# Kernel tuning notes

Hardware: AMD Instinct MI355X
Metric: run time of the kernel (lower is better)

## Reference

```python
import jax, jax.numpy as jnp
import numpy as np

MARGIN = 0.5

def setup_inputs() -> dict:
    key = jax.random.key(0)
    k1, k2 = jax.random.split(key)
    inputs = jax.random.normal(k1, (8192, 256), dtype=jnp.float32)
    target = jax.random.randint(k2, (8192,), 0, 100, dtype=jnp.int64)
    return {"inputs": inputs, "target": target}

def reference(inputs, target):
    N = inputs.shape[0]
    # pairwise squared distances via ||xi||^2 + ||xj||^2 - 2 xi.xj
    sq = jnp.sum(inputs * inputs, axis=1)  # [N]
    gram = inputs @ inputs.T               # [N, N]
    distance = sq[:, None] + sq[None, :] - 2.0 * gram  # [N, N]
    R = (target[None, :] == target[:, None]).astype(inputs.dtype)  # [N, N]
    loss = R * distance + (1.0 - R) * jnp.maximum(MARGIN - distance, 0.0)
    return jnp.sum(loss) / (N * (N - 1.0) * 2.0)
```

## Files before the change

kernel.cpp:

```cpp
#include <hip/hip_runtime.h>
#include <stdint.h>

#define N      8192
#define KDIM   256
#define BM     128
#define TILES  (N / BM)
#define NPAIRS (TILES * (TILES + 1) / 2)
#define MARGIN 0.5f
#define PLANE  ((size_t)N * 128)

typedef float     f32x4 __attribute__((ext_vector_type(4)));
typedef long long i64x2 __attribute__((ext_vector_type(2)));

__device__ __forceinline__ void async_copy16(const void* g, void* l) {
    __builtin_amdgcn_global_load_lds(
        (__attribute__((address_space(1))) void*)(g),
        (__attribute__((address_space(3))) void*)(l),
        16, 0, 0);
}

#if !__has_builtin(__builtin_amdgcn_cvt_pk_fp8_f32)
__device__ __forceinline__ uint32_t f2e4m3(float f) {
    uint32_t u = __float_as_uint(f);
    uint32_t s = (u >> 24) & 0x80u;
    uint32_t au = u & 0x7fffffffu;
    if (au == 0) return s;
    int32_t  exp = (int32_t)(au >> 23) - 127;
    uint32_t man = (au & 0x7fffffu) | 0x800000u;
    uint32_t code;
    if (exp >= -6) {
        code = (uint32_t)((exp + 7) << 3) | ((man >> 20) & 7u);
        uint32_t rem = man & 0xFFFFFu;
        if (rem > 0x80000u || (rem == 0x80000u && (code & 1u))) code++;
    } else {
        int shift = 14 - exp;
        if (shift > 24) return s;
        code = man >> shift;
        uint32_t rem = man & ((1u << shift) - 1u);
        uint32_t h = 1u << (shift - 1);
        if (rem > h || (rem == h && (code & 1u))) code++;
    }
    return s | code;
}
__device__ __forceinline__ uint32_t pack_fp8x4(float4 v) {
    return f2e4m3(v.x) | (f2e4m3(v.y) << 8) | (f2e4m3(v.z) << 16) |
           (f2e4m3(v.w) << 24);
}
#else
__device__ __forceinline__ uint32_t pack_fp8x4(float4 v) {
    int pk = __builtin_amdgcn_cvt_pk_fp8_f32(v.x, v.y, 0, false);
    pk = __builtin_amdgcn_cvt_pk_fp8_f32(v.z, v.w, pk, true);
    return (uint32_t)pk;
}
#endif

__global__ __launch_bounds__(256) void prep_kernel(
        const float* __restrict__ X, uint8_t* __restrict__ Xq,
        float* __restrict__ sq) {
    int row  = blockIdx.x * 4 + (threadIdx.x >> 6);
    int lane = threadIdx.x & 63;

    float4 v = *((const float4*)(X + (size_t)row * KDIM) + lane);
    float ss = v.x * v.x + v.y * v.y + v.z * v.z + v.w * v.w;
    uint32_t pk = pack_fp8x4(v);

    int kg = lane * 4;
    int h  = kg >> 7;
    int kh = kg & 127;
    int ks = kh >> 5;
    int fq = (kh >> 3) & 3;
    int slot = (fq * 2 + (ks >> 1)) ^ (row & 7);
    size_t off = (size_t)h * PLANE + (size_t)row * 128
               + slot * 16 + (ks & 1) * 8 + (kh & 4);
    *(uint32_t*)(Xq + off) = pk;

    #pragma unroll
    for (int o = 32; o > 0; o >>= 1) ss += __shfl_down(ss, o, 64);
    if (lane == 0) sq[row] = ss;
}

__device__ __forceinline__ void compute_half(
        const uint8_t* aB, const uint8_t* bB, int fquad, int key,
        f32x4 (&acc)[4][4]) {
    #pragma unroll
    for (int ks2 = 0; ks2 < 2; ++ks2) {
        const int t = ((fquad * 2 + ks2) ^ key) * 16;
        i64x2 a2[4], b2[4];
        #pragma unroll
        for (int im = 0; im < 4; ++im)
            a2[im] = *(const i64x2*)(aB + im * 16 * 128 + t);
        #pragma unroll
        for (int in = 0; in < 4; ++in)
            b2[in] = *(const i64x2*)(bB + in * 16 * 128 + t);
        #pragma unroll
        for (int im = 0; im < 4; ++im)
            #pragma unroll
            for (int in = 0; in < 4; ++in)
                acc[im][in] = __builtin_amdgcn_mfma_f32_16x16x32_fp8_fp8(
                    a2[im].x, b2[in].x, acc[im][in], 0, 0, 0);
        #pragma unroll
        for (int im = 0; im < 4; ++im)
            #pragma unroll
            for (int in = 0; in < 4; ++in)
                acc[im][in] = __builtin_amdgcn_mfma_f32_16x16x32_fp8_fp8(
                    a2[im].y, b2[in].y, acc[im][in], 0, 0, 0);
    }
}

__global__ __launch_bounds__(256, 2) void loss_kernel(
        const uint8_t* __restrict__ Xq, const float* __restrict__ sq,
        const int* __restrict__ tgt, float* __restrict__ partials) {
    const int p = blockIdx.x;
    float tf = 2.0f * TILES + 1.0f;
    int bi = (int)((tf - sqrtf(tf * tf - 8.0f * (float)p)) * 0.5f);
    if (bi < 0) bi = 0;
    while (bi > 0 && (bi * TILES - bi * (bi - 1) / 2) > p) --bi;
    while (((bi + 1) * TILES - (bi + 1) * bi / 2) <= p) ++bi;
    const int bj = bi + (p - (bi * TILES - bi * (bi - 1) / 2));

    __shared__ __align__(16) uint8_t As0[BM * 128];
    __shared__ __align__(16) uint8_t As1[BM * 128];
    __shared__ __align__(16) uint8_t Bs0[BM * 128];
    __shared__ __align__(16) uint8_t Bs1[BM * 128];
    __shared__ float sqa_s[BM], sqb_s[BM];
    __shared__ int   ta_s[BM],  tb_s[BM];
    __shared__ float wsum[4];

    const int tid  = threadIdx.x;
    const int wave = tid >> 6;
    const int lane = tid & 63;

    if (tid < 128) {
        sqa_s[tid] = sq[bi * BM + tid];
        ta_s[tid]  = tgt[bi * BM + tid];
    } else {
        int r = tid - 128;
        sqb_s[r] = sq[bj * BM + r];
        tb_s[r]  = tgt[bj * BM + r];
    }

    const int lrow = lane >> 3;
    const int lb   = (lane & 7) * 16;
    const uint8_t* gA0 = Xq + ((size_t)bi * BM + wave * 32 + lrow) * 128 + lb;
    const uint8_t* gB0 = Xq + ((size_t)bj * BM + wave * 32 + lrow) * 128 + lb;
    uint8_t* lA0 = As0 + wave * 32 * 128;
    uint8_t* lB0 = Bs0 + wave * 32 * 128;
    uint8_t* lA1 = As1 + wave * 32 * 128;
    uint8_t* lB1 = Bs1 + wave * 32 * 128;

    #pragma unroll
    for (int q = 0; q < 4; ++q) {
        async_copy16(gA0 + q * 8 * 128, lA0 + q * 1024);
        async_copy16(gB0 + q * 8 * 128, lB0 + q * 1024);
    }
    #pragma unroll
    for (int q = 0; q < 4; ++q) {
        async_copy16(gA0 + PLANE + q * 8 * 128, lA1 + q * 1024);
        async_copy16(gB0 + PLANE + q * 8 * 128, lB1 + q * 1024);
    }

    const int frow  = lane & 15;
    const int fquad = lane >> 4;
    const int wm = (wave >> 1) * 64;
    const int wn = (wave & 1) * 64;
    const int key = frow & 7;

    f32x4 acc[4][4];
    #pragma unroll
    for (int im = 0; im < 4; ++im)
        #pragma unroll
        for (int in = 0; in < 4; ++in)
            acc[im][in] = (f32x4){0.f, 0.f, 0.f, 0.f};

    asm volatile("s_waitcnt vmcnt(8) lgkmcnt(0)" ::: "memory");
    __builtin_amdgcn_s_barrier();

    compute_half(As0 + (wm + frow) * 128, Bs0 + (wn + frow) * 128,
                 fquad, key, acc);

    asm volatile("s_waitcnt vmcnt(0)" ::: "memory");
    __builtin_amdgcn_s_barrier();

    compute_half(As1 + (wm + frow) * 128, Bs1 + (wn + frow) * 128,
                 fquad, key, acc);

    float lsum = 0.0f;
    if (bi != bj) {
        #pragma unroll
        for (int im = 0; im < 4; ++im) {
            #pragma unroll
            for (int in = 0; in < 4; ++in) {
                #pragma unroll
                for (int r = 0; r < 4; ++r) {
                    int rl = wm + im * 16 + fquad * 4 + r;
                    int cl = wn + in * 16 + frow;
                    float d = fmaf(-2.0f, acc[im][in][r],
                                   sqa_s[rl] + sqb_s[cl]);
                    lsum += (ta_s[rl] == tb_s[cl]) ? d
                                                   : fmaxf(MARGIN - d, 0.0f);
                }
            }
        }
        lsum *= 2.0f;
    } else {
        #pragma unroll
        for (int im = 0; im < 4; ++im) {
            #pragma unroll
            for (int in = 0; in < 4; ++in) {
                #pragma unroll
                for (int r = 0; r < 4; ++r) {
                    int rl = wm + im * 16 + fquad * 4 + r;
                    int cl = wn + in * 16 + frow;
                    float d = fmaf(-2.0f, acc[im][in][r],
                                   sqa_s[rl] + sqb_s[cl]);
                    float c = (ta_s[rl] == tb_s[cl]) ? d
                                                     : fmaxf(MARGIN - d, 0.0f);
                    float w = (rl < cl) ? 2.0f : ((rl == cl) ? 1.0f : 0.0f);
                    lsum += w * c;
                }
            }
        }
    }

    #pragma unroll
    for (int o = 32; o > 0; o >>= 1) lsum += __shfl_down(lsum, o, 64);
    if (lane == 0) wsum[wave] = lsum;
    __syncthreads();
    if (tid == 0) partials[p] = wsum[0] + wsum[1] + wsum[2] + wsum[3];
}

__global__ __launch_bounds__(256) void reduce_kernel(
        const float* __restrict__ partials, float* __restrict__ out,
        int n, float scale) {
    float s = 0.0f;
    for (int i = threadIdx.x; i < n; i += 256) s += partials[i];
    __shared__ float w[4];
    #pragma unroll
    for (int o = 32; o > 0; o >>= 1) s += __shfl_down(s, o, 64);
    int wave = threadIdx.x >> 6, lane = threadIdx.x & 63;
    if (lane == 0) w[wave] = s;
    __syncthreads();
    if (threadIdx.x == 0) out[0] = (w[0] + w[1] + w[2] + w[3]) * scale;
}

extern "C" void kernel_launch(void* const* d_in, const int* in_sizes, int n_in,
                              void* d_out, int out_size, void* d_ws, size_t ws_size,
                              hipStream_t stream) {
    (void)in_sizes; (void)n_in; (void)out_size; (void)ws_size;
    const float* X   = (const float*)d_in[0];
    const int*   tgt = (const int*)d_in[1];

    uint8_t* Xq     = (uint8_t*)d_ws;
    float* sq       = (float*)((char*)d_ws + (size_t)N * KDIM);
    float* partials = sq + N;

    prep_kernel<<<N / 4, 256, 0, stream>>>(X, Xq, sq);
    loss_kernel<<<NPAIRS, 256, 0, stream>>>(Xq, sq, tgt, partials);

    const float scale = (float)(1.0 / ((double)N * ((double)N - 1.0) * 2.0));
    reduce_kernel<<<1, 256, 0, stream>>>(partials, (float*)d_out, NPAIRS, scale);
}
```

Baseline: 85.29 us.

## Single-buffer LDS with interleaved FP8 rows to raise blocks per CU

```diff
diff --git a/kernel.cpp b/kernel.cpp
--- a/kernel.cpp
+++ b/kernel.cpp
@@ -7,7 +7,6 @@
 #define TILES  (N / BM)
 #define NPAIRS (TILES * (TILES + 1) / 2)
 #define MARGIN 0.5f
-#define PLANE  ((size_t)N * 128)
 
 typedef float     f32x4 __attribute__((ext_vector_type(4)));
 typedef long long i64x2 __attribute__((ext_vector_type(2)));
@@ -70,8 +69,7 @@
     int ks = kh >> 5;
     int fq = (kh >> 3) & 3;
     int slot = (fq * 2 + (ks >> 1)) ^ (row & 7);
-    size_t off = (size_t)h * PLANE + (size_t)row * 128
-               + slot * 16 + (ks & 1) * 8 + (kh & 4);
+    size_t off = (size_t)row * 256 + h * 128 + slot * 16 + (ks & 1) * 8 + (kh & 4);
     *(uint32_t*)(Xq + off) = pk;
 
     #pragma unroll
@@ -79,35 +77,7 @@
     if (lane == 0) sq[row] = ss;
 }
 
-__device__ __forceinline__ void compute_half(
-        const uint8_t* aB, const uint8_t* bB, int fquad, int key,
-        f32x4 (&acc)[4][4]) {
-    #pragma unroll
-    for (int ks2 = 0; ks2 < 2; ++ks2) {
-        const int t = ((fquad * 2 + ks2) ^ key) * 16;
-        i64x2 a2[4], b2[4];
-        #pragma unroll
-        for (int im = 0; im < 4; ++im)
-            a2[im] = *(const i64x2*)(aB + im * 16 * 128 + t);
-        #pragma unroll
-        for (int in = 0; in < 4; ++in)
-            b2[in] = *(const i64x2*)(bB + in * 16 * 128 + t);
-        #pragma unroll
-        for (int im = 0; im < 4; ++im)
-            #pragma unroll
-            for (int in = 0; in < 4; ++in)
-                acc[im][in] = __builtin_amdgcn_mfma_f32_16x16x32_fp8_fp8(
-                    a2[im].x, b2[in].x, acc[im][in], 0, 0, 0);
-        #pragma unroll
-        for (int im = 0; im < 4; ++im)
-            #pragma unroll
-            for (int in = 0; in < 4; ++in)
-                acc[im][in] = __builtin_amdgcn_mfma_f32_16x16x32_fp8_fp8(
-                    a2[im].y, b2[in].y, acc[im][in], 0, 0, 0);
-    }
-}
-
-__global__ __launch_bounds__(256, 2) void loss_kernel(
+__global__ __launch_bounds__(256, 4) void loss_kernel(
         const uint8_t* __restrict__ Xq, const float* __restrict__ sq,
         const int* __restrict__ tgt, float* __restrict__ partials) {
     const int p = blockIdx.x;
@@ -118,10 +88,8 @@
     while (((bi + 1) * TILES - (bi + 1) * bi / 2) <= p) ++bi;
     const int bj = bi + (p - (bi * TILES - bi * (bi - 1) / 2));
 
-    __shared__ __align__(16) uint8_t As0[BM * 128];
-    __shared__ __align__(16) uint8_t As1[BM * 128];
-    __shared__ __align__(16) uint8_t Bs0[BM * 128];
-    __shared__ __align__(16) uint8_t Bs1[BM * 128];
+    __shared__ __align__(16) uint8_t As[BM * 128];
+    __shared__ __align__(16) uint8_t Bs[BM * 128];
     __shared__ float sqa_s[BM], sqb_s[BM];
     __shared__ int   ta_s[BM],  tb_s[BM];
     __shared__ float wsum[4];
@@ -141,29 +109,18 @@
 
     const int lrow = lane >> 3;
     const int lb   = (lane & 7) * 16;
-    const uint8_t* gA0 = Xq + ((size_t)bi * BM + wave * 32 + lrow) * 128 + lb;
-    const uint8_t* gB0 = Xq + ((size_t)bj * BM + wave * 32 + lrow) * 128 + lb;
-    uint8_t* lA0 = As0 + wave * 32 * 128;
-    uint8_t* lB0 = Bs0 + wave * 32 * 128;
-    uint8_t* lA1 = As1 + wave * 32 * 128;
-    uint8_t* lB1 = Bs1 + wave * 32 * 128;
-
-    #pragma unroll
-    for (int q = 0; q < 4; ++q) {
-        async_copy16(gA0 + q * 8 * 128, lA0 + q * 1024);
-        async_copy16(gB0 + q * 8 * 128, lB0 + q * 1024);
-    }
-    #pragma unroll
-    for (int q = 0; q < 4; ++q) {
-        async_copy16(gA0 + PLANE + q * 8 * 128, lA1 + q * 1024);
-        async_copy16(gB0 + PLANE + q * 8 * 128, lB1 + q * 1024);
-    }
+    const uint8_t* gA0 = Xq + ((size_t)bi * BM + wave * 32 + lrow) * 256 + lb;
+    const uint8_t* gB0 = Xq + ((size_t)bj * BM + wave * 32 + lrow) * 256 + lb;
+    uint8_t* lA = As + wave * 32 * 128;
+    uint8_t* lB = Bs + wave * 32 * 128;
 
     const int frow  = lane & 15;
     const int fquad = lane >> 4;
     const int wm = (wave >> 1) * 64;
     const int wn = (wave & 1) * 64;
     const int key = frow & 7;
+    const uint8_t* aB = As + (wm + frow) * 128;
+    const uint8_t* bB = Bs + (wn + frow) * 128;
 
     f32x4 acc[4][4];
     #pragma unroll
@@ -172,32 +129,60 @@
         for (int in = 0; in < 4; ++in)
             acc[im][in] = (f32x4){0.f, 0.f, 0.f, 0.f};
 
-    asm volatile("s_waitcnt vmcnt(8) lgkmcnt(0)" ::: "memory");
-    __builtin_amdgcn_s_barrier();
-
-    compute_half(As0 + (wm + frow) * 128, Bs0 + (wn + frow) * 128,
-                 fquad, key, acc);
-
-    asm volatile("s_waitcnt vmcnt(0)" ::: "memory");
-    __builtin_amdgcn_s_barrier();
-
-    compute_half(As1 + (wm + frow) * 128, Bs1 + (wn + frow) * 128,
-                 fquad, key, acc);
+    #pragma unroll
+    for (int h = 0; h < 2; ++h) {
+        #pragma unroll
+        for (int q = 0; q < 4; ++q) {
+            async_copy16(gA0 + h * 128 + q * 8 * 256, lA + q * 1024);
+            async_copy16(gB0 + h * 128 + q * 8 * 256, lB + q * 1024);
+        }
+        __syncthreads();
+
+        #pragma unroll
+        for (int ks2 = 0; ks2 < 2; ++ks2) {
+            const int t = ((fquad * 2 + ks2) ^ key) * 16;
+            i64x2 a2[4], b2[4];
+            #pragma unroll
+            for (int im = 0; im < 4; ++im)
+                a2[im] = *(const i64x2*)(aB + im * 16 * 128 + t);
+            #pragma unroll
+            for (int in = 0; in < 4; ++in)
+                b2[in] = *(const i64x2*)(bB + in * 16 * 128 + t);
+            #pragma unroll
+            for (int im = 0; im < 4; ++im)
+                #pragma unroll
+                for (int in = 0; in < 4; ++in)
+                    acc[im][in] = __builtin_amdgcn_mfma_f32_16x16x32_fp8_fp8(
+                        a2[im].x, b2[in].x, acc[im][in], 0, 0, 0);
+            #pragma unroll
+            for (int im = 0; im < 4; ++im)
+                #pragma unroll
+                for (int in = 0; in < 4; ++in)
+                    acc[im][in] = __builtin_amdgcn_mfma_f32_16x16x32_fp8_fp8(
+                        a2[im].y, b2[in].y, acc[im][in], 0, 0, 0);
+        }
+        if (h == 0) __syncthreads();
+    }
+
+    float sqb_r[4]; int tb_r[4];
+    #pragma unroll
+    for (int in = 0; in < 4; ++in) {
+        sqb_r[in] = sqb_s[wn + in * 16 + frow];
+        tb_r[in]  = tb_s[wn + in * 16 + frow];
+    }
 
     float lsum = 0.0f;
     if (bi != bj) {
         #pragma unroll
         for (int im = 0; im < 4; ++im) {
             #pragma unroll
-            for (int in = 0; in < 4; ++in) {
-                #pragma unroll
-                for (int r = 0; r < 4; ++r) {
-                    int rl = wm + im * 16 + fquad * 4 + r;
-                    int cl = wn + in * 16 + frow;
-                    float d = fmaf(-2.0f, acc[im][in][r],
-                                   sqa_s[rl] + sqb_s[cl]);
-                    lsum += (ta_s[rl] == tb_s[cl]) ? d
-                                                   : fmaxf(MARGIN - d, 0.0f);
+            for (int r = 0; r < 4; ++r) {
+                int rl = wm + im * 16 + fquad * 4 + r;
+                float sqa = sqa_s[rl]; int ta = ta_s[rl];
+                #pragma unroll
+                for (int in = 0; in < 4; ++in) {
+                    float d = fmaf(-2.0f, acc[im][in][r], sqa + sqb_r[in]);
+                    lsum += (ta == tb_r[in]) ? d : fmaxf(MARGIN - d, 0.0f);
                 }
             }
         }
@@ -206,15 +191,14 @@
         #pragma unroll
         for (int im = 0; im < 4; ++im) {
             #pragma unroll
-            for (int in = 0; in < 4; ++in) {
-                #pragma unroll
-                for (int r = 0; r < 4; ++r) {
-                    int rl = wm + im * 16 + fquad * 4 + r;
+            for (int r = 0; r < 4; ++r) {
+                int rl = wm + im * 16 + fquad * 4 + r;
+                float sqa = sqa_s[rl]; int ta = ta_s[rl];
+                #pragma unroll
+                for (int in = 0; in < 4; ++in) {
                     int cl = wn + in * 16 + frow;
-                    float d = fmaf(-2.0f, acc[im][in][r],
-                                   sqa_s[rl] + sqb_s[cl]);
-                    float c = (ta_s[rl] == tb_s[cl]) ? d
-                                                     : fmaxf(MARGIN - d, 0.0f);
+                    float d = fmaf(-2.0f, acc[im][in][r], sqa + sqb_r[in]);
+                    float c = (ta == tb_r[in]) ? d : fmaxf(MARGIN - d, 0.0f);
                     float w = (rl < cl) ? 2.0f : ((rl == cl) ? 1.0f : 0.0f);
                     lsum += w * c;
                 }
```

Result: faster. 79.73 us (-6.5%).
